# Kernel tuning notes

Hardware: AMD Instinct MI355X
Metric: run time of the kernel (lower is better)

Reference implementation:

```python
import jax, jax.numpy as jnp
import numpy as np

N_WIRES = 4
N_REUP = 3
N_Q_LAYERS = 2
SEQ_LEN = 10
GRU_HIDDEN = 16


def setup_inputs() -> dict:
    key = jax.random.key(0)
    ks = jax.random.split(key, 24)
    N, E = 10000, 320000
    s = 0.25
    inp = {
        'x': jax.random.normal(ks[0], (N, SEQ_LEN + 3), jnp.float32),
        'edge_index': jax.random.randint(ks[1], (2, E), 0, N, dtype=jnp.int32),
        'edge_attr': jax.random.normal(ks[2], (E, 1), jnp.float32),
        'W_ih': jax.random.normal(ks[3], (3 * GRU_HIDDEN, 1), jnp.float32) * s,
        'W_hh': jax.random.normal(ks[4], (3 * GRU_HIDDEN, GRU_HIDDEN), jnp.float32) * s,
        'b_ih': jax.random.normal(ks[5], (3 * GRU_HIDDEN,), jnp.float32) * s,
        'b_hh': jax.random.normal(ks[6], (3 * GRU_HIDDEN,), jnp.float32) * s,
        'p1_W': jax.random.normal(ks[7], (N_WIRES, GRU_HIDDEN + 3), jnp.float32) * s,
        'p1_b': jax.random.normal(ks[8], (N_WIRES,), jnp.float32) * s,
        'a1_W': jax.random.normal(ks[9], (1, 2 * N_WIRES), jnp.float32) * s,
        'q1_w': jax.random.uniform(ks[10], (N_REUP, N_Q_LAYERS, 2), jnp.float32, -np.pi, np.pi),
        'g1': jnp.ones((N_WIRES,), jnp.float32),
        'be1': jnp.zeros((N_WIRES,), jnp.float32),
        'p2_W': jax.random.normal(ks[11], (N_WIRES, N_WIRES), jnp.float32) * s,
        'p2_b': jax.random.normal(ks[12], (N_WIRES,), jnp.float32) * s,
        'a2_W': jax.random.normal(ks[13], (1, 2 * N_WIRES), jnp.float32) * s,
        'q2_w': jax.random.uniform(ks[14], (N_REUP, N_Q_LAYERS, 2), jnp.float32, -np.pi, np.pi),
        'g2': jnp.ones((N_WIRES,), jnp.float32),
        'be2': jnp.zeros((N_WIRES,), jnp.float32),
        'r_W': jax.random.normal(ks[15], (1, N_WIRES), jnp.float32) * s,
        'r_b': jax.random.normal(ks[16], (1,), jnp.float32) * s,
    }
    return inp


def _ry(theta):
    c = jnp.cos(theta * 0.5)
    s = jnp.sin(theta * 0.5)
    return jnp.stack([jnp.stack([c, -s], -1), jnp.stack([s, c], -1)], -2).astype(jnp.complex64)


def _rz(theta):
    em = jnp.exp(-0.5j * theta)
    ep = jnp.exp(0.5j * theta)
    z = jnp.zeros_like(em)
    return jnp.stack([jnp.stack([em, z], -1), jnp.stack([z, ep], -1)], -2)


def _apply1q(state, gate, wire):
    # state: [E,2,2,2,2]; gate: [2,2] shared or [E,2,2] per-edge
    st = jnp.moveaxis(state, 1 + wire, -1)
    if gate.ndim == 3:
        st = jnp.einsum('eij,e...j->e...i', gate, st)
    else:
        st = jnp.einsum('ij,e...j->e...i', gate, st)
    return jnp.moveaxis(st, -1, 1 + wire)


def _cnot(state, c, t):
    st = jnp.moveaxis(state, (1 + c, 1 + t), (-2, -1))
    st = jnp.concatenate([st[..., :1, :], st[..., 1:, ::-1]], axis=-2)
    return jnp.moveaxis(st, (-2, -1), (1 + c, 1 + t))


def _qcircuit(inputs, corr, weights):
    # inputs: [E,4] angles, corr: [E], weights: [3,2,2]; batched 4-wire statevector sim
    E = inputs.shape[0]
    state = jnp.zeros((E, 16), jnp.complex64).at[:, 0].set(1.0).reshape(E, 2, 2, 2, 2)
    for r in range(N_REUP):
        for i in range(N_WIRES):
            state = _apply1q(state, _ry(inputs[:, i]), i)
        state = _apply1q(state, _ry(corr), 0)
        for d in range(N_Q_LAYERS):
            gy = _ry(weights[r, d, 0])
            gz = _rz(weights[r, d, 1])
            for i in range(N_WIRES):
                state = _apply1q(state, gy, i)
                state = _apply1q(state, gz, i)
            for i in range(d % 2, N_WIRES - 1, 2):
                state = _cnot(state, i, i + 1)
    probs = state.real ** 2 + state.imag ** 2
    z = jnp.array([1.0, -1.0], jnp.float32)
    return jnp.stack(
        [jnp.einsum('e...j,j->e', jnp.moveaxis(probs, 1 + w, -1), z) for w in range(N_WIRES)], -1)


def _layernorm(x, g, b):
    mu = x.mean(-1, keepdims=True)
    v = ((x - mu) ** 2).mean(-1, keepdims=True)
    return (x - mu) * jax.lax.rsqrt(v + 1e-5) * g + b


def _qgat(x, edge_index, edge_attr, Wp, bp, Wa, qw, g, b):
    N = x.shape[0]
    h = jax.nn.elu(x @ Wp.T + bp)  # [N,4]
    sl = jnp.arange(N, dtype=edge_index.dtype)
    src = jnp.concatenate([edge_index[0], sl])
    dst = jnp.concatenate([edge_index[1], sl])
    ea = jnp.concatenate([edge_attr[:, 0], jnp.ones((N,), x.dtype)])
    alpha = jnp.concatenate([h[src], h[dst]], -1) @ Wa[0]  # [Et]
    alpha = jax.nn.leaky_relu(alpha, 0.2) * jnp.abs(ea)
    alpha = alpha - jax.lax.stop_gradient(alpha).max()
    aexp = jnp.exp(alpha)
    dsum = jax.ops.segment_sum(aexp, dst, num_segments=N)
    alpha = aexp / (dsum[dst] + 1e-8)
    corr = jnp.tanh(ea) * jnp.pi
    msg = alpha[:, None] * _qcircuit(jnp.tanh(h[src]) * jnp.pi, corr, qw)  # [Et,4]
    aggr = jax.ops.segment_sum(msg, dst, num_segments=N)
    return _layernorm(aggr + h, g, b)


def _gru_last(price_seq, W_ih, W_hh, b_ih, b_hh):
    # price_seq: [N,T] scalar-per-step GRU; returns final hidden [N,H]
    N = price_seq.shape[0]
    h0 = jnp.zeros((N, GRU_HIDDEN), price_seq.dtype)
    w_in = W_ih[:, 0]  # [3H]

    def step(h, x_t):
        gi = x_t[:, None] * w_in + b_ih  # [N,3H]
        gh = h @ W_hh.T + b_hh
        ir, iz, inn = jnp.split(gi, 3, -1)
        hr, hz, hn = jnp.split(gh, 3, -1)
        r = jax.nn.sigmoid(ir + hr)
        z = jax.nn.sigmoid(iz + hz)
        n = jnp.tanh(inn + r * hn)
        return (1.0 - z) * n + z * h, None

    h, _ = jax.lax.scan(step, h0, price_seq.T)
    return h


def reference(x, edge_index, edge_attr, W_ih, W_hh, b_ih, b_hh,
              p1_W, p1_b, a1_W, q1_w, g1, be1,
              p2_W, p2_b, a2_W, q2_w, g2, be2, r_W, r_b):
    hT = _gru_last(x[:, :SEQ_LEN], W_ih, W_hh, b_ih, b_hh)
    h = jnp.concatenate([hT, x[:, SEQ_LEN:]], -1)  # [N,19]
    h = jax.nn.relu(_qgat(h, edge_index, edge_attr, p1_W, p1_b, a1_W, q1_w, g1, be1))
    h = _qgat(h, edge_index, edge_attr, p2_W, p2_b, a2_W, q2_w, g2, be2)
    return (h @ r_W.T + r_b)[:, 0]
```

## Files before the change

kernel.cpp:

```cpp
#include <hip/hip_runtime.h>
#include <math.h>


#define GH 16
#define SEQ 10
#define PI_F 3.14159265358979323846f

__device__ __forceinline__ float sigmoidf_(float x) { return 1.0f / (1.0f + expf(-x)); }

template <int STR>
__device__ __forceinline__ void ry_g(float (&sr)[16], float (&si)[16], float c, float s) {
#pragma unroll
    for (int i0 = 0; i0 < 16; ++i0) {
        if (i0 & STR) continue;
        int i1 = i0 | STR;
        float a0r = sr[i0], a0i = si[i0], a1r = sr[i1], a1i = si[i1];
        sr[i0] = c * a0r - s * a1r; si[i0] = c * a0i - s * a1i;
        sr[i1] = s * a0r + c * a1r; si[i1] = s * a0i + c * a1i;
    }
}
template <int STR>
__device__ __forceinline__ void rz_g(float (&sr)[16], float (&si)[16], float c, float s) {
#pragma unroll
    for (int i = 0; i < 16; ++i) {
        float r = sr[i], im = si[i];
        if (i & STR) { sr[i] = r * c - im * s; si[i] = im * c + r * s; }
        else         { sr[i] = r * c + im * s; si[i] = im * c - r * s; }
    }
}
template <int SC, int ST>
__device__ __forceinline__ void cnot_g(float (&sr)[16], float (&si)[16]) {
#pragma unroll
    for (int i = 0; i < 16; ++i) {
        if ((i & SC) && !(i & ST)) {
            int j = i | ST;
            float tr = sr[i], ti = si[i];
            sr[i] = sr[j]; si[i] = si[j]; sr[j] = tr; si[j] = ti;
        }
    }
}

__global__ __launch_bounds__(128) void k_gmat(
    const float* __restrict__ q1w, const float* __restrict__ q2w,
    float* __restrict__ Gtab)
{
    int t = threadIdx.x;
    if (t >= 96) return;
    int layer = t / 48, rem = t % 48, rep = rem / 16, col = rem % 16;
    const float* qw = layer ? q2w : q1w;
    float sr[16], si[16];
#pragma unroll
    for (int i = 0; i < 16; ++i) { sr[i] = 0.f; si[i] = 0.f; }
    sr[col] = 1.f;
#pragma unroll
    for (int d = 0; d < 2; ++d) {
        float cy, sy, cz, sz;
        sincosf(0.5f * qw[(rep * 2 + d) * 2 + 0], &sy, &cy);
        sincosf(0.5f * qw[(rep * 2 + d) * 2 + 1], &sz, &cz);
        bool lastd = (rep == 2) && (d == 1);
        ry_g<8>(sr, si, cy, sy); if (!lastd) rz_g<8>(sr, si, cz, sz);
        ry_g<4>(sr, si, cy, sy); if (!lastd) rz_g<4>(sr, si, cz, sz);
        ry_g<2>(sr, si, cy, sy); if (!lastd) rz_g<2>(sr, si, cz, sz);
        ry_g<1>(sr, si, cy, sy); if (!lastd) rz_g<1>(sr, si, cz, sz);
        if (d == 0) { cnot_g<8, 4>(sr, si); cnot_g<2, 1>(sr, si); }
        else        { cnot_g<4, 2>(sr, si); }
    }
    float* g = Gtab + layer * 1536 + rep * 512;
#pragma unroll
    for (int i = 0; i < 16; ++i) {
        g[(i * 16 + col) * 2 + 0] = sr[i];
        g[(i * 16 + col) * 2 + 1] = si[i];
    }
}

__device__ __forceinline__ void prep_node(
    int lane, int n, float c0, float s0, float c1, float s1,
    float c2, float s2, float c3, float s3, float hsd,
    const float (&gr)[3][16 * 17], const float (&gi)[3][16 * 17],
    float* __restrict__ T)
{
    float pa = (lane & 8) ? 0.f
             : ((lane & 4) ? s1 : c1) * ((lane & 2) ? s2 : c2) * ((lane & 1) ? s3 : c3);
    float pb;
    { float t = __shfl_xor(pa, 8, 16); pb = (lane & 8) ? t : -t; }

    float ar = 0.f, ai = 0.f, br = 0.f, bi = 0.f;
#pragma unroll
    for (int jj = 0; jj < 16; ++jj) {
        float Gr = gr[0][lane * 17 + jj], Gi = gi[0][lane * 17 + jj];
        float xa = __shfl(pa, jj, 16), xb = __shfl(pb, jj, 16);
        ar += Gr * xa; ai += Gi * xa; br += Gr * xb; bi += Gi * xb;
    }

#define BFLY(vr, vi, STR, cc, ss) { \
    float tr_ = __shfl_xor(vr, STR, 16), ti_ = __shfl_xor(vi, STR, 16); \
    float sg_ = (lane & STR) ? (ss) : -(ss); \
    vr = (cc) * vr + sg_ * tr_; vi = (cc) * vi + sg_ * ti_; }
#define R123(vr, vi) { BFLY(vr, vi, 4, c1, s1) BFLY(vr, vi, 2, c2, s2) BFLY(vr, vi, 1, c3, s3) }
#define KAPP(orr, oii, xr, xi) { \
    float tr_ = __shfl_xor(xr, 8, 16), ti_ = __shfl_xor(xi, 8, 16); \
    orr = (lane & 8) ? tr_ : -tr_; oii = (lane & 8) ? ti_ : -ti_; }

    R123(ar, ai) R123(br, bi)

    float sr4[4], si4[4];
    sr4[0] = ar; si4[0] = ai;
    KAPP(sr4[1], si4[1], ar, ai)
    sr4[2] = br; si4[2] = bi;
    KAPP(sr4[3], si4[3], br, bi)

    float nr4[4] = {0.f, 0.f, 0.f, 0.f}, ni4[4] = {0.f, 0.f, 0.f, 0.f};
#pragma unroll
    for (int jj = 0; jj < 16; ++jj) {
        float Gr = gr[1][lane * 17 + jj], Gi = gi[1][lane * 17 + jj];
#pragma unroll
        for (int v = 0; v < 4; ++v) {
            float xr = __shfl(sr4[v], jj, 16), xi = __shfl(si4[v], jj, 16);
            nr4[v] += Gr * xr - Gi * xi;
            ni4[v] += Gr * xi + Gi * xr;
        }
    }
#pragma unroll
    for (int v = 0; v < 4; ++v) { R123(nr4[v], ni4[v]) }

    float gr4[4], gi4[4];
    float m01r = nr4[1] + nr4[2], m01i = ni4[1] + ni4[2];
    gr4[0] = nr4[0]; gi4[0] = ni4[0];
    { float kr, ki; KAPP(kr, ki, nr4[0], ni4[0]) gr4[1] = m01r + kr; gi4[1] = m01i + ki; }
    { float kr, ki; KAPP(kr, ki, m01r, m01i)     gr4[2] = nr4[3] + kr; gi4[2] = ni4[3] + ki; }
    { float kr, ki; KAPP(kr, ki, nr4[3], ni4[3]) gr4[3] = kr; gi4[3] = ki; }

    float vr4[4] = {0.f, 0.f, 0.f, 0.f}, vi4[4] = {0.f, 0.f, 0.f, 0.f};
#pragma unroll
    for (int jj = 0; jj < 16; ++jj) {
        float Gr = gr[2][lane * 17 + jj], Gi = gi[2][lane * 17 + jj];
#pragma unroll
        for (int v = 0; v < 4; ++v) {
            float xr = __shfl(gr4[v], jj, 16), xi = __shfl(gi4[v], jj, 16);
            vr4[v] += Gr * xr - Gi * xi;
            vi4[v] += Gr * xi + Gi * xr;
        }
    }

    float p[10];
    {
        int idx = 0;
#pragma unroll
        for (int k = 0; k < 4; ++k)
#pragma unroll
            for (int l = 0; l < 4; ++l) {
                if (l < k) continue;
                p[idx++] = vr4[k] * vr4[l] + vi4[k] * vi4[l];
            }
    }
#pragma unroll
    for (int pi = 0; pi < 10; ++pi) {
        float v = p[pi];
#pragma unroll
        for (int m = 8; m >= 1; m >>= 1) {
            float t = __shfl_xor(v, m, 16);
            v = (lane & m) ? (t - v) : (v + t);
        }
        p[pi] = v;
    }

    float* Tb = T + (size_t)n * 48;
    int w = (lane == 8) ? 0 : (lane == 4) ? 1 : (lane == 2) ? 2 : (lane == 1) ? 3 : -1;
    if (w >= 0) {
#pragma unroll
        for (int pi = 0; pi < 10; ++pi) {
            float mult = (pi == 0 || pi == 4 || pi == 7 || pi == 9) ? 1.f : 2.f;
            Tb[w * 10 + pi] = mult * p[pi];
        }
    }
    if (lane == 0) { Tb[40] = c0; Tb[41] = s0; Tb[42] = hsd; Tb[43] = 0.f; }
#undef BFLY
#undef R123
#undef KAPP
}

__global__ __launch_bounds__(256) void k_gru(
    const float* __restrict__ x, const float* __restrict__ W_ih,
    const float* __restrict__ W_hh, const float* __restrict__ b_ih,
    const float* __restrict__ b_hh, const float* __restrict__ p1W,
    const float* __restrict__ p1b, const float* __restrict__ a1W,
    const float* __restrict__ Gl, const int* __restrict__ ei,
    int* __restrict__ deg, float* __restrict__ nres1,
    float* __restrict__ hdd1, float* __restrict__ T,
    float* __restrict__ Sz, int N, int E)
{
    for (int i = blockIdx.x * 256 + threadIdx.x; i < N * 10; i += gridDim.x * 256)
        Sz[i] = 0.f;
    for (int e = blockIdx.x * 256 + threadIdx.x; e < E; e += gridDim.x * 256)
        atomicAdd(&deg[ei[E + e]], 1);

    __shared__ float sW[48 * 16];
    __shared__ float sp1W[4 * 19], sp1b[4];
    __shared__ float gr[3][16 * 17], gi[3][16 * 17];
    for (int i = threadIdx.x; i < 48 * 16; i += 256) sW[i] = W_hh[i];
    if (threadIdx.x < 76) sp1W[threadIdx.x] = p1W[threadIdx.x];
    if (threadIdx.x < 4) sp1b[threadIdx.x] = p1b[threadIdx.x];
    for (int idx = threadIdx.x; idx < 3 * 256; idx += 256) {
        int rep = idx >> 8, rc = idx & 255, i = rc >> 4, jj = rc & 15;
        gr[rep][i * 17 + jj] = Gl[rep * 512 + rc * 2 + 0];
        gi[rep][i * 17 + jj] = Gl[rep * 512 + rc * 2 + 1];
    }
    __syncthreads();

    const int j = threadIdx.x & 15;
    const int n = blockIdx.x * 16 + (threadIdx.x >> 4);
    const bool valid = (n < N);

    float wr[GH], wz[GH], wn[GH];
#pragma unroll
    for (int k = 0; k < GH; ++k) {
        wr[k] = sW[j * 16 + k];
        wz[k] = sW[(16 + j) * 16 + k];
        wn[k] = sW[(32 + j) * 16 + k];
    }
    float wir = W_ih[j], wiz = W_ih[16 + j], win_ = W_ih[32 + j];
    float bir = b_ih[j], biz = b_ih[16 + j], bin_ = b_ih[32 + j];
    float brr = b_hh[j], brz = b_hh[16 + j], brn = b_hh[32 + j];

    float xv[13];
#pragma unroll
    for (int t = 0; t < 13; ++t) xv[t] = valid ? x[n * 13 + t] : 0.f;

    float h = 0.f;
#pragma unroll
    for (int t = 0; t < SEQ; ++t) {
        float xt = xv[t];
        float ghr = brr, ghz = brz, ghn = brn;
#pragma unroll
        for (int k = 0; k < GH; ++k) {
            float hk = __shfl(h, k, 16);
            ghr += wr[k] * hk; ghz += wz[k] * hk; ghn += wn[k] * hk;
        }
        float r  = sigmoidf_(xt * wir + bir + ghr);
        float z  = sigmoidf_(xt * wiz + biz + ghz);
        float nv = tanhf(xt * win_ + bin_ + r * ghn);
        h = (1.f - z) * nv + z * h;
    }

    float b0 = h * sp1W[0 * 19 + j];
    float b1 = h * sp1W[1 * 19 + j];
    float b2 = h * sp1W[2 * 19 + j];
    float b3 = h * sp1W[3 * 19 + j];
#pragma unroll
    for (int m = 1; m < 16; m <<= 1) {
        b0 += __shfl_xor(b0, m, 16);
        b1 += __shfl_xor(b1, m, 16);
        b2 += __shfl_xor(b2, m, 16);
        b3 += __shfl_xor(b3, m, 16);
    }

    float hv = 0.f, cv = 1.f, sv = 0.f, ds = 0.f, dd = 0.f;
    if (j < 4) {
        float s = (j == 0) ? b0 : (j == 1) ? b1 : (j == 2) ? b2 : b3;
        s += sp1b[j] + xv[10] * sp1W[j * 19 + 16] + xv[11] * sp1W[j * 19 + 17]
           + xv[12] * sp1W[j * 19 + 18];
        hv = (s > 0.f) ? s : expm1f(s);
        sincosf(0.5f * PI_F * tanhf(hv), &sv, &cv);
        ds = hv * a1W[j];
        dd = hv * a1W[4 + j];
    }
    ds += __shfl_xor(ds, 1, 16); ds += __shfl_xor(ds, 2, 16);
    dd += __shfl_xor(dd, 1, 16); dd += __shfl_xor(dd, 2, 16);

    float c0 = __shfl(cv, 0, 16), s0 = __shfl(sv, 0, 16);
    float c1 = __shfl(cv, 1, 16), s1 = __shfl(sv, 1, 16);
    float c2 = __shfl(cv, 2, 16), s2 = __shfl(sv, 2, 16);
    float c3 = __shfl(cv, 3, 16), s3 = __shfl(sv, 3, 16);
    float hsd = __shfl(ds, 0, 16);

    if (valid) {
        if (j < 4) nres1[n * 4 + j] = hv;
        if (j == 0) hdd1[n] = dd;
        prep_node(j, n, c0, s0, c1, s1, c2, s2, c3, s3, hsd, gr, gi, T);
    }
}

__global__ __launch_bounds__(1024) void k_scan(
    const int* __restrict__ deg, int* __restrict__ off,
    int* __restrict__ cur, int N)
{
    __shared__ int part[1024];
    const int t = threadIdx.x;
    const int chunk = (N + 1023) / 1024;
    const int lo = t * chunk;
    const int hi = min(lo + chunk, N);
    int s = 0;
    for (int i = lo; i < hi; ++i) s += deg[i] + 1;
    part[t] = s;
    __syncthreads();
    for (int d = 1; d < 1024; d <<= 1) {
        int y = (t >= d) ? part[t - d] : 0;
        __syncthreads();
        part[t] += y;
        __syncthreads();
    }
    int run = part[t] - s;
    for (int i = lo; i < hi; ++i) { off[i] = run; cur[i] = run; run += deg[i] + 1; }
}

__global__ __launch_bounds__(256) void k_fill(
    const int* __restrict__ ei, const float* __restrict__ ea,
    int* __restrict__ cur, float4* __restrict__ rec, int E, int N)
{
    int idx = blockIdx.x * 256 + threadIdx.x;
    if (idx >= E + N) return;
    int src, d; float ev;
    if (idx < E) { src = ei[idx]; d = ei[E + idx]; ev = ea[idx]; }
    else         { src = idx - E; d = src;         ev = 1.0f;    }
    int slot = atomicAdd(&cur[d], 1);
    float scv, ccv; sincosf(0.5f * PI_F * tanhf(ev), &scv, &ccv);
    float4 r;
    r.x = __int_as_float(src | (d << 16));
    r.y = fabsf(ev);
    r.z = ccv; r.w = scv;
    rec[slot] = r;
}

__device__ __forceinline__ void segreduce(
    int dst, int lane, float a0, float a1, float a2, float a3, float a4,
    float* __restrict__ S)
{
    int prevd = __shfl_up(dst, 1);
    bool head = (lane == 0) || (prevd != dst);
    unsigned long long hm = __ballot(head);
    unsigned long long below = (2ull << lane) - 1ull;
    int H = 63 - __clzll((long long)(hm & below));
    int dist = lane - H;
#pragma unroll
    for (int st = 1; st < 64; st <<= 1) {
        float t0 = __shfl_up(a0, st), t1 = __shfl_up(a1, st),
              t2 = __shfl_up(a2, st), t3 = __shfl_up(a3, st),
              t4 = __shfl_up(a4, st);
        if (dist >= st) { a0 += t0; a1 += t1; a2 += t2; a3 += t3; a4 += t4; }
    }
    int nextd = __shfl_down(dst, 1);
    bool lastl = (lane == 63) || (dst != nextd);
    if (lastl && dst >= 0) {
        float* sbase = S + (size_t)dst * 5;
        atomicAdd(sbase + 0, a0); atomicAdd(sbase + 1, a1);
        atomicAdd(sbase + 2, a2); atomicAdd(sbase + 3, a3);
        atomicAdd(sbase + 4, a4);
    }
}

__global__ __launch_bounds__(256) void k_edge(
    const float4* __restrict__ rec, const float* __restrict__ T,
    const float* __restrict__ hdd, float* __restrict__ S, int EN)
{
    const int slot = blockIdx.x * 256 + threadIdx.x;
    const int lane = threadIdx.x & 63;
    int dst = -1;
    float acc0 = 0.f, acc1 = 0.f, acc2 = 0.f, acc3 = 0.f, acc4 = 0.f;

    if (slot < EN) {
        float4 r = rec[slot];
        int ids = __float_as_int(r.x);
        int src = ids & 0xFFFF;
        dst = ids >> 16;
        float aea = r.y, ccv = r.z, scv = r.w;

        const float* Tb = T + (size_t)src * 48;
        float t[44];
#pragma unroll
        for (int q = 0; q < 11; ++q) {
            float4 v4 = *reinterpret_cast<const float4*>(Tb + q * 4);
            t[q * 4 + 0] = v4.x; t[q * 4 + 1] = v4.y;
            t[q * 4 + 2] = v4.z; t[q * 4 + 3] = v4.w;
        }
        float hdN = hdd[dst];

        float mc = t[40] * ccv - t[41] * scv;
        float ms = t[41] * ccv + t[40] * scv;
        float m2 = mc * mc, s2 = ms * ms;
        float cf0 = mc * m2, cf1 = m2 * ms, cf2 = mc * s2, cf3 = ms * s2;
        float qq[10];
        qq[0] = cf0 * cf0; qq[1] = cf0 * cf1; qq[2] = cf0 * cf2; qq[3] = cf0 * cf3;
        qq[4] = cf1 * cf1; qq[5] = cf1 * cf2; qq[6] = cf1 * cf3;
        qq[7] = cf2 * cf2; qq[8] = cf2 * cf3; qq[9] = cf3 * cf3;

        float z0 = 0.f, z1 = 0.f, z2 = 0.f, z3 = 0.f;
#pragma unroll
        for (int pi = 0; pi < 10; ++pi) {
            z0 += t[pi] * qq[pi];
            z1 += t[10 + pi] * qq[pi];
            z2 += t[20 + pi] * qq[pi];
            z3 += t[30 + pi] * qq[pi];
        }

        float s0a = t[42] + hdN;
        s0a = (s0a > 0.f) ? s0a : 0.2f * s0a;
        float aexp = expf(s0a * aea);
        acc0 = aexp * z0; acc1 = aexp * z1; acc2 = aexp * z2; acc3 = aexp * z3;
        acc4 = aexp;
    }
    segreduce(dst, lane, acc0, acc1, acc2, acc3, acc4, S);
}

__global__ __launch_bounds__(256) void k_nodeprep(
    const float* __restrict__ S, const float* __restrict__ nres,
    const float* __restrict__ g4, const float* __restrict__ be4,
    const float* __restrict__ pW, const float* __restrict__ pb,
    const float* __restrict__ WaN, const float* __restrict__ Gl,
    float* __restrict__ onres, float* __restrict__ ohdd,
    float* __restrict__ T, int N)
{
    __shared__ float gr[3][16 * 17], gi[3][16 * 17];
    for (int idx = threadIdx.x; idx < 3 * 256; idx += 256) {
        int rep = idx >> 8, rc = idx & 255, i = rc >> 4, jj = rc & 15;
        gr[rep][i * 17 + jj] = Gl[rep * 512 + rc * 2 + 0];
        gi[rep][i * 17 + jj] = Gl[rep * 512 + rc * 2 + 1];
    }
    __syncthreads();

    const int lane = threadIdx.x & 15;
    const int n = blockIdx.x * 16 + (threadIdx.x >> 4);
    if (n >= N) return;

    const float* sb = S + (size_t)n * 5;
    float dn = sb[4] + 1e-8f;
    float v0 = sb[0] / dn + nres[n * 4 + 0];
    float v1 = sb[1] / dn + nres[n * 4 + 1];
    float v2 = sb[2] / dn + nres[n * 4 + 2];
    float v3 = sb[3] / dn + nres[n * 4 + 3];
    float mu = 0.25f * (v0 + v1 + v2 + v3);
    float d0 = v0 - mu, d1 = v1 - mu, d2 = v2 - mu, d3 = v3 - mu;
    float var = 0.25f * (d0 * d0 + d1 * d1 + d2 * d2 + d3 * d3);
    float rs = 1.0f / sqrtf(var + 1e-5f);
    float y0 = fmaxf(d0 * rs * g4[0] + be4[0], 0.f);
    float y1 = fmaxf(d1 * rs * g4[1] + be4[1], 0.f);
    float y2 = fmaxf(d2 * rs * g4[2] + be4[2], 0.f);
    float y3 = fmaxf(d3 * rs * g4[3] + be4[3], 0.f);

    float hv[4];
#pragma unroll
    for (int w = 0; w < 4; ++w) {
        float s = pb[w] + y0 * pW[w * 4 + 0] + y1 * pW[w * 4 + 1]
                + y2 * pW[w * 4 + 2] + y3 * pW[w * 4 + 3];
        hv[w] = (s > 0.f) ? s : expm1f(s);
    }

    float cv = 1.f, sv = 0.f;
    if (lane < 4) sincosf(0.5f * PI_F * tanhf(hv[lane]), &sv, &cv);
    float c0 = __shfl(cv, 0, 16), s0 = __shfl(sv, 0, 16);
    float c1 = __shfl(cv, 1, 16), s1 = __shfl(sv, 1, 16);
    float c2 = __shfl(cv, 2, 16), s2 = __shfl(sv, 2, 16);
    float c3 = __shfl(cv, 3, 16), s3 = __shfl(sv, 3, 16);

    float hsd = hv[0] * WaN[0] + hv[1] * WaN[1] + hv[2] * WaN[2] + hv[3] * WaN[3];
    if (lane < 4) onres[n * 4 + lane] = hv[lane];
    if (lane == 0)
        ohdd[n] = hv[0] * WaN[4] + hv[1] * WaN[5] + hv[2] * WaN[6] + hv[3] * WaN[7];

    prep_node(lane, n, c0, s0, c1, s1, c2, s2, c3, s3, hsd, gr, gi, T);
}

__global__ __launch_bounds__(256) void k_node2(
    const float* __restrict__ S, const float* __restrict__ nres,
    const float* __restrict__ g4, const float* __restrict__ be4,
    const float* __restrict__ rW, const float* __restrict__ rb,
    float* __restrict__ out, int N)
{
    int n = blockIdx.x * 256 + threadIdx.x;
    if (n >= N) return;
    const float* sb = S + (size_t)n * 5;
    float dn = sb[4] + 1e-8f;
    float v0 = sb[0] / dn + nres[n * 4 + 0];
    float v1 = sb[1] / dn + nres[n * 4 + 1];
    float v2 = sb[2] / dn + nres[n * 4 + 2];
    float v3 = sb[3] / dn + nres[n * 4 + 3];
    float mu = 0.25f * (v0 + v1 + v2 + v3);
    float d0 = v0 - mu, d1 = v1 - mu, d2 = v2 - mu, d3 = v3 - mu;
    float var = 0.25f * (d0 * d0 + d1 * d1 + d2 * d2 + d3 * d3);
    float rs = 1.0f / sqrtf(var + 1e-5f);
    out[n] = rb[0]
           + (d0 * rs * g4[0] + be4[0]) * rW[0]
           + (d1 * rs * g4[1] + be4[1]) * rW[1]
           + (d2 * rs * g4[2] + be4[2]) * rW[2]
           + (d3 * rs * g4[3] + be4[3]) * rW[3];
}

extern "C" void kernel_launch(void* const* d_in, const int* in_sizes, int n_in,
                              void* d_out, int out_size, void* d_ws, size_t ws_size,
                              hipStream_t stream)
{
    const float* x    = (const float*)d_in[0];
    const int*   ei   = (const int*)d_in[1];
    const float* ea   = (const float*)d_in[2];
    const float* W_ih = (const float*)d_in[3];
    const float* W_hh = (const float*)d_in[4];
    const float* b_ih = (const float*)d_in[5];
    const float* b_hh = (const float*)d_in[6];
    const float* p1W  = (const float*)d_in[7];
    const float* p1b  = (const float*)d_in[8];
    const float* a1W  = (const float*)d_in[9];
    const float* q1w  = (const float*)d_in[10];
    const float* g1   = (const float*)d_in[11];
    const float* be1  = (const float*)d_in[12];
    const float* p2W  = (const float*)d_in[13];
    const float* p2b  = (const float*)d_in[14];
    const float* a2W  = (const float*)d_in[15];
    const float* q2w  = (const float*)d_in[16];
    const float* g2   = (const float*)d_in[17];
    const float* be2  = (const float*)d_in[18];
    const float* rW   = (const float*)d_in[19];
    const float* rb   = (const float*)d_in[20];
    float* out = (float*)d_out;

    int N  = in_sizes[0] / 13;
    int E  = in_sizes[1] / 2;
    int EN = E + N;

    float* ws    = (float*)d_ws;
    float* nres1 = ws;
    float* nres2 = nres1 + (size_t)N * 4;
    float* hdd1  = nres2 + (size_t)N * 4;
    float* hdd2  = hdd1 + N;
    float* S1    = hdd2 + N;
    float* S2    = S1 + (size_t)N * 5;
    float* Gtab  = S2 + (size_t)N * 5;
    float* T     = Gtab + 3072;
    int* deg  = (int*)(T + (size_t)N * 48);
    int* off  = deg + N;
    int* cur  = off + N;
    uintptr_t rp = (uintptr_t)(cur + N);
    rp = (rp + 15u) & ~(uintptr_t)15u;
    float4* rec = (float4*)rp;

    hipMemsetAsync(deg, 0, (size_t)N * sizeof(int), stream);

    const int B = 256;
    k_gmat<<<1, 128, 0, stream>>>(q1w, q2w, Gtab);
    k_gru<<<(N + 15) / 16, B, 0, stream>>>(x, W_ih, W_hh, b_ih, b_hh, p1W, p1b,
                                           a1W, Gtab, ei, deg, nres1, hdd1, T,
                                           S1, N, E);
    k_scan<<<1, 1024, 0, stream>>>(deg, off, cur, N);
    k_fill<<<(EN + B - 1) / B, B, 0, stream>>>(ei, ea, cur, rec, E, N);

    k_edge<<<(EN + B - 1) / B, B, 0, stream>>>(rec, T, hdd1, S1, EN);
    k_nodeprep<<<(N + 15) / 16, B, 0, stream>>>(
        S1, nres1, g1, be1, p2W, p2b, a2W, Gtab + 1536, nres2, hdd2, T, N);

    k_edge<<<(EN + B - 1) / B, B, 0, stream>>>(rec, T, hdd2, S2, EN);
    k_node2<<<(N + B - 1) / B, B, 0, stream>>>(S2, nres2, g2, be2, rW, rb, out, N);
}
```

Measured before the change: 232.8 us.

## Split GRU matvec across 32 lanes per node and stage T output in shared memory

k_gru now assigns 32 lanes per node instead of 16, so each half-group computes half of the 16-term recurrent dot product and the halves are combined with a cross-half shuffle. This shortens the serial dependency chain in each GRU step. Both k_gru and k_nodeprep now write the per-node T records to shared memory first and then copy them to global memory in one coalesced block store. The W_hh shared array is padded to avoid bank conflicts. The cost is twice as many blocks, a second block-wide sync, and half the lanes sitting idle during prep_node.

```diff
diff --git a/kernel.cpp b/kernel.cpp
--- a/kernel.cpp
+++ b/kernel.cpp
@@ -74,10 +74,10 @@
 }
 
 __device__ __forceinline__ void prep_node(
-    int lane, int n, float c0, float s0, float c1, float s1,
+    int lane, float c0, float s0, float c1, float s1,
     float c2, float s2, float c3, float s3, float hsd,
     const float (&gr)[3][16 * 17], const float (&gi)[3][16 * 17],
-    float* __restrict__ T)
+    float* __restrict__ Tb)
 {
     float pa = (lane & 8) ? 0.f
              : ((lane & 4) ? s1 : c1) * ((lane & 2) ? s2 : c2) * ((lane & 1) ? s3 : c3);
@@ -164,7 +164,6 @@
         p[pi] = v;
     }
 
-    float* Tb = T + (size_t)n * 48;
     int w = (lane == 8) ? 0 : (lane == 4) ? 1 : (lane == 2) ? 2 : (lane == 1) ? 3 : -1;
     if (w >= 0) {
 #pragma unroll
@@ -194,10 +193,12 @@
     for (int e = blockIdx.x * 256 + threadIdx.x; e < E; e += gridDim.x * 256)
         atomicAdd(&deg[ei[E + e]], 1);
 
-    __shared__ float sW[48 * 16];
+    __shared__ float sW[48 * 17];
     __shared__ float sp1W[4 * 19], sp1b[4];
     __shared__ float gr[3][16 * 17], gi[3][16 * 17];
-    for (int i = threadIdx.x; i < 48 * 16; i += 256) sW[i] = W_hh[i];
+    __shared__ float sT[8 * 48];
+    for (int i = threadIdx.x; i < 48 * 16; i += 256)
+        sW[(i >> 4) * 17 + (i & 15)] = W_hh[i];
     if (threadIdx.x < 76) sp1W[threadIdx.x] = p1W[threadIdx.x];
     if (threadIdx.x < 4) sp1b[threadIdx.x] = p1b[threadIdx.x];
     for (int idx = threadIdx.x; idx < 3 * 256; idx += 256) {
@@ -207,16 +208,20 @@
     }
     __syncthreads();
 
-    const int j = threadIdx.x & 15;
-    const int n = blockIdx.x * 16 + (threadIdx.x >> 4);
+    const int L = threadIdx.x & 31;
+    const int j = L & 15;
+    const int half = L >> 4;
+    const int nib = threadIdx.x >> 5;
+    const int n = blockIdx.x * 8 + nib;
     const bool valid = (n < N);
 
-    float wr[GH], wz[GH], wn[GH];
-#pragma unroll
-    for (int k = 0; k < GH; ++k) {
-        wr[k] = sW[j * 16 + k];
-        wz[k] = sW[(16 + j) * 16 + k];
-        wn[k] = sW[(32 + j) * 16 + k];
+    float wr8[8], wz8[8], wn8[8];
+#pragma unroll
+    for (int kk = 0; kk < 8; ++kk) {
+        int k = half * 8 + kk;
+        wr8[kk] = sW[j * 17 + k];
+        wz8[kk] = sW[(16 + j) * 17 + k];
+        wn8[kk] = sW[(32 + j) * 17 + k];
     }
     float wir = W_ih[j], wiz = W_ih[16 + j], win_ = W_ih[32 + j];
     float bir = b_ih[j], biz = b_ih[16 + j], bin_ = b_ih[32 + j];
@@ -230,15 +235,18 @@
 #pragma unroll
     for (int t = 0; t < SEQ; ++t) {
         float xt = xv[t];
-        float ghr = brr, ghz = brz, ghn = brn;
-#pragma unroll
-        for (int k = 0; k < GH; ++k) {
-            float hk = __shfl(h, k, 16);
-            ghr += wr[k] * hk; ghz += wz[k] * hk; ghn += wn[k] * hk;
-        }
-        float r  = sigmoidf_(xt * wir + bir + ghr);
-        float z  = sigmoidf_(xt * wiz + biz + ghz);
-        float nv = tanhf(xt * win_ + bin_ + r * ghn);
+        float pr = 0.f, pz = 0.f, pn = 0.f;
+#pragma unroll
+        for (int kk = 0; kk < 8; ++kk) {
+            float hk = __shfl(h, half * 8 + kk, 16);
+            pr += wr8[kk] * hk; pz += wz8[kk] * hk; pn += wn8[kk] * hk;
+        }
+        pr += __shfl_xor(pr, 16, 32);
+        pz += __shfl_xor(pz, 16, 32);
+        pn += __shfl_xor(pn, 16, 32);
+        float r  = sigmoidf_(xt * wir + bir + brr + pr);
+        float z  = sigmoidf_(xt * wiz + biz + brz + pz);
+        float nv = tanhf(xt * win_ + bin_ + r * (brn + pn));
         h = (1.f - z) * nv + z * h;
     }
 
@@ -274,9 +282,17 @@
     float hsd = __shfl(ds, 0, 16);
 
     if (valid) {
-        if (j < 4) nres1[n * 4 + j] = hv;
-        if (j == 0) hdd1[n] = dd;
-        prep_node(j, n, c0, s0, c1, s1, c2, s2, c3, s3, hsd, gr, gi, T);
+        if (L < 4) nres1[n * 4 + L] = hv;
+        if (L == 0) hdd1[n] = dd;
+    }
+    if (L < 16)
+        prep_node(j, c0, s0, c1, s1, c2, s2, c3, s3, hsd, gr, gi, sT + nib * 48);
+    __syncthreads();
+    {
+        int n0 = blockIdx.x * 8;
+        int cnt = (min(n0 + 8, N) - n0) * 48;
+        for (int i = threadIdx.x; i < cnt; i += 256)
+            T[(size_t)n0 * 48 + i] = sT[i];
     }
 }
 
@@ -410,6 +426,7 @@
     float* __restrict__ T, int N)
 {
     __shared__ float gr[3][16 * 17], gi[3][16 * 17];
+    __shared__ float sT[8 * 48];
     for (int idx = threadIdx.x; idx < 3 * 256; idx += 256) {
         int rep = idx >> 8, rc = idx & 255, i = rc >> 4, jj = rc & 15;
         gr[rep][i * 17 + jj] = Gl[rep * 512 + rc * 2 + 0];
@@ -417,46 +434,58 @@
     }
     __syncthreads();
 
-    const int lane = threadIdx.x & 15;
-    const int n = blockIdx.x * 16 + (threadIdx.x >> 4);
-    if (n >= N) return;
-
-    const float* sb = S + (size_t)n * 5;
-    float dn = sb[4] + 1e-8f;
-    float v0 = sb[0] / dn + nres[n * 4 + 0];
-    float v1 = sb[1] / dn + nres[n * 4 + 1];
-    float v2 = sb[2] / dn + nres[n * 4 + 2];
-    float v3 = sb[3] / dn + nres[n * 4 + 3];
-    float mu = 0.25f * (v0 + v1 + v2 + v3);
-    float d0 = v0 - mu, d1 = v1 - mu, d2 = v2 - mu, d3 = v3 - mu;
-    float var = 0.25f * (d0 * d0 + d1 * d1 + d2 * d2 + d3 * d3);
-    float rs = 1.0f / sqrtf(var + 1e-5f);
-    float y0 = fmaxf(d0 * rs * g4[0] + be4[0], 0.f);
-    float y1 = fmaxf(d1 * rs * g4[1] + be4[1], 0.f);
-    float y2 = fmaxf(d2 * rs * g4[2] + be4[2], 0.f);
-    float y3 = fmaxf(d3 * rs * g4[3] + be4[3], 0.f);
-
-    float hv[4];
-#pragma unroll
-    for (int w = 0; w < 4; ++w) {
-        float s = pb[w] + y0 * pW[w * 4 + 0] + y1 * pW[w * 4 + 1]
-                + y2 * pW[w * 4 + 2] + y3 * pW[w * 4 + 3];
-        hv[w] = (s > 0.f) ? s : expm1f(s);
+    const int L = threadIdx.x & 31;
+    const int j = L & 15;
+    const int nib = threadIdx.x >> 5;
+    const int n = blockIdx.x * 8 + nib;
+    const bool valid = (n < N);
+
+    float hv[4] = {0.f, 0.f, 0.f, 0.f};
+    if (valid) {
+        const float* sb = S + (size_t)n * 5;
+        float dn = sb[4] + 1e-8f;
+        float v0 = sb[0] / dn + nres[n * 4 + 0];
+        float v1 = sb[1] / dn + nres[n * 4 + 1];
+        float v2 = sb[2] / dn + nres[n * 4 + 2];
+        float v3 = sb[3] / dn + nres[n * 4 + 3];
+        float mu = 0.25f * (v0 + v1 + v2 + v3);
+        float d0 = v0 - mu, d1 = v1 - mu, d2 = v2 - mu, d3 = v3 - mu;
+        float var = 0.25f * (d0 * d0 + d1 * d1 + d2 * d2 + d3 * d3);
+        float rs = 1.0f / sqrtf(var + 1e-5f);
+        float y0 = fmaxf(d0 * rs * g4[0] + be4[0], 0.f);
+        float y1 = fmaxf(d1 * rs * g4[1] + be4[1], 0.f);
+        float y2 = fmaxf(d2 * rs * g4[2] + be4[2], 0.f);
+        float y3 = fmaxf(d3 * rs * g4[3] + be4[3], 0.f);
+#pragma unroll
+        for (int w = 0; w < 4; ++w) {
+            float s = pb[w] + y0 * pW[w * 4 + 0] + y1 * pW[w * 4 + 1]
+                    + y2 * pW[w * 4 + 2] + y3 * pW[w * 4 + 3];
+            hv[w] = (s > 0.f) ? s : expm1f(s);
+        }
     }
 
     float cv = 1.f, sv = 0.f;
-    if (lane < 4) sincosf(0.5f * PI_F * tanhf(hv[lane]), &sv, &cv);
+    if (j < 4) sincosf(0.5f * PI_F * tanhf(hv[j]), &sv, &cv);
     float c0 = __shfl(cv, 0, 16), s0 = __shfl(sv, 0, 16);
     float c1 = __shfl(cv, 1, 16), s1 = __shfl(sv, 1, 16);
     float c2 = __shfl(cv, 2, 16), s2 = __shfl(sv, 2, 16);
     float c3 = __shfl(cv, 3, 16), s3 = __shfl(sv, 3, 16);
 
     float hsd = hv[0] * WaN[0] + hv[1] * WaN[1] + hv[2] * WaN[2] + hv[3] * WaN[3];
-    if (lane < 4) onres[n * 4 + lane] = hv[lane];
-    if (lane == 0)
-        ohdd[n] = hv[0] * WaN[4] + hv[1] * WaN[5] + hv[2] * WaN[6] + hv[3] * WaN[7];
-
-    prep_node(lane, n, c0, s0, c1, s1, c2, s2, c3, s3, hsd, gr, gi, T);
+    if (valid) {
+        if (L < 4) onres[n * 4 + L] = hv[L];
+        if (L == 0)
+            ohdd[n] = hv[0] * WaN[4] + hv[1] * WaN[5] + hv[2] * WaN[6] + hv[3] * WaN[7];
+    }
+    if (L < 16)
+        prep_node(j, c0, s0, c1, s1, c2, s2, c3, s3, hsd, gr, gi, sT + nib * 48);
+    __syncthreads();
+    {
+        int n0 = blockIdx.x * 8;
+        int cnt = (min(n0 + 8, N) - n0) * 48;
+        for (int i = threadIdx.x; i < cnt; i += 256)
+            T[(size_t)n0 * 48 + i] = sT[i];
+    }
 }
 
 __global__ __launch_bounds__(256) void k_node2(
@@ -535,14 +564,14 @@
 
     const int B = 256;
     k_gmat<<<1, 128, 0, stream>>>(q1w, q2w, Gtab);
-    k_gru<<<(N + 15) / 16, B, 0, stream>>>(x, W_ih, W_hh, b_ih, b_hh, p1W, p1b,
-                                           a1W, Gtab, ei, deg, nres1, hdd1, T,
-                                           S1, N, E);
+    k_gru<<<(N + 7) / 8, B, 0, stream>>>(x, W_ih, W_hh, b_ih, b_hh, p1W, p1b,
+                                         a1W, Gtab, ei, deg, nres1, hdd1, T,
+                                         S1, N, E);
     k_scan<<<1, 1024, 0, stream>>>(deg, off, cur, N);
     k_fill<<<(EN + B - 1) / B, B, 0, stream>>>(ei, ea, cur, rec, E, N);
 
     k_edge<<<(EN + B - 1) / B, B, 0, stream>>>(rec, T, hdd1, S1, EN);
-    k_nodeprep<<<(N + 15) / 16, B, 0, stream>>>(
+    k_nodeprep<<<(N + 7) / 8, B, 0, stream>>>(
         S1, nres1, g1, be1, p2W, p2b, a2W, Gtab + 1536, nres2, hdd2, T, N);
 
     k_edge<<<(EN + B - 1) / B, B, 0, stream>>>(rec, T, hdd2, S2, EN);
```

New measurement: 244.8 us. 5.2% more time.
